# Kernel optimization log

Measured on AMD Instinct MI355X. Metric: run time of the kernel, lower is better.

Reference implementation:

```python
import jax, jax.numpy as jnp
import numpy as np

N = 100000
E = 1600000
F_IN = 32
HID = 16
C_OUT = 10
K = 4


def setup_inputs() -> dict:
    key = jax.random.key(0)
    k1, k2, k3, k4, k5, k6, k7 = jax.random.split(key, 7)
    x = jax.random.normal(k1, (N, F_IN), dtype=jnp.float32)
    edge_index = jax.random.randint(k2, (2, E), 0, N, dtype=jnp.int64)
    # ChebConv weights: one [in, out] matrix per Chebyshev order k
    W1 = jax.random.normal(k3, (K, F_IN, HID), dtype=jnp.float32) / np.sqrt(F_IN)
    b1 = jax.random.normal(k4, (HID,), dtype=jnp.float32) * 0.01
    W2 = jax.random.normal(k5, (K, HID, C_OUT), dtype=jnp.float32) / np.sqrt(HID)
    b2 = jax.random.normal(k6, (C_OUT,), dtype=jnp.float32) * 0.01
    return {"x": x, "edge_index": edge_index, "W1": W1, "b1": b1, "W2": W2, "b2": b2}


def _cheb_conv(h, src, dst, norm, W, b, num_nodes):
    # Tx_0 = h; Tx_1 = L_hat h; Tx_k = 2 L_hat Tx_{k-1} - Tx_{k-2}
    def prop(v):  # v: [N, F] -> L_hat v via sparse gather/scatter
        return jax.ops.segment_sum(norm[:, None] * v[src], dst, num_segments=num_nodes)

    Tx0 = h
    out = Tx0 @ W[0]
    Tx1 = prop(h)
    out = out + Tx1 @ W[1]
    for k in range(2, W.shape[0]):
        Tx2 = 2.0 * prop(Tx1) - Tx0
        out = out + Tx2 @ W[k]
        Tx0, Tx1 = Tx1, Tx2
    return out + b


def reference(x, edge_index, W1, b1, W2, b2):
    src, dst = edge_index[0], edge_index[1]
    num_nodes = x.shape[0]
    # symmetric normalization with lambda_max = 2: L_hat = -D^{-1/2} A D^{-1/2}
    deg = jax.ops.segment_sum(jnp.ones((src.shape[0],), dtype=x.dtype), dst, num_segments=num_nodes)
    dis = jnp.where(deg > 0, jax.lax.rsqrt(jnp.maximum(deg, 1.0)), 0.0)
    norm = -dis[src] * dis[dst]
    h = _cheb_conv(x, src, dst, norm, W1, b1, num_nodes)
    h = jax.nn.relu(h)
    # dropout is identity in eval mode
    h = _cheb_conv(h, src, dst, norm, W2, b2, num_nodes)
    return jax.nn.log_softmax(h, axis=1)
```

## Files before the change

kernel.cpp:

```cpp
#include <hip/hip_runtime.h>
#include <hip/hip_bf16.h>
#include <math.h>


#define BLK 256
#define BLKP 512
#define NBUCK_MAX 256
#define CHUNK 4096
#define CAPB 16384
#define PLACE_CAP 10240

__device__ inline unsigned short f32_to_bf16_rne(float f) {
    unsigned int u = __float_as_uint(f);
    unsigned int rounding = 0x7FFFu + ((u >> 16) & 1u);
    return (unsigned short)((u + rounding) >> 16);
}
__device__ inline unsigned int pack_bf16x2(float a, float b) {
    return (unsigned int)f32_to_bf16_rne(a) | ((unsigned int)f32_to_bf16_rne(b) << 16);
}
__device__ inline void unpack8(const uint4 u, float* f) {
    const unsigned int* p = &u.x;
#pragma unroll
    for (int j = 0; j < 4; j++) {
        unsigned int w = p[j];
        f[2 * j]     = __uint_as_float(w << 16);
        f[2 * j + 1] = __uint_as_float(w & 0xFFFF0000u);
    }
}
__device__ inline void add8(const uint4 u, float* acc) {
    const unsigned int* p = &u.x;
#pragma unroll
    for (int j = 0; j < 4; j++) {
        unsigned int w = p[j];
        acc[2 * j]     += __uint_as_float(w << 16);
        acc[2 * j + 1] += __uint_as_float(w & 0xFFFF0000u);
    }
}
__device__ inline uint4 pack8(const float* r) {
    uint4 o;
    o.x = pack_bf16x2(r[0], r[1]);
    o.y = pack_bf16x2(r[2], r[3]);
    o.z = pack_bf16x2(r[4], r[5]);
    o.w = pack_bf16x2(r[6], r[7]);
    return o;
}

__device__ inline void gather_sum(const int* __restrict__ psrc, int b, int e,
                                  const uint4* __restrict__ vb, int c, float* acc) {
    int i = b;
    for (; i + 7 < e; i += 8) {
        int s0 = psrc[i],     s1 = psrc[i + 1], s2 = psrc[i + 2], s3 = psrc[i + 3];
        int s4 = psrc[i + 4], s5 = psrc[i + 5], s6 = psrc[i + 6], s7 = psrc[i + 7];
        uint4 a0 = vb[(size_t)s0 * 2 + c];
        uint4 a1 = vb[(size_t)s1 * 2 + c];
        uint4 a2 = vb[(size_t)s2 * 2 + c];
        uint4 a3 = vb[(size_t)s3 * 2 + c];
        uint4 a4 = vb[(size_t)s4 * 2 + c];
        uint4 a5 = vb[(size_t)s5 * 2 + c];
        uint4 a6 = vb[(size_t)s6 * 2 + c];
        uint4 a7 = vb[(size_t)s7 * 2 + c];
        add8(a0, acc); add8(a1, acc); add8(a2, acc); add8(a3, acc);
        add8(a4, acc); add8(a5, acc); add8(a6, acc); add8(a7, acc);
    }
    for (; i + 3 < e; i += 4) {
        int s0 = psrc[i], s1 = psrc[i + 1], s2 = psrc[i + 2], s3 = psrc[i + 3];
        uint4 a0 = vb[(size_t)s0 * 2 + c];
        uint4 a1 = vb[(size_t)s1 * 2 + c];
        uint4 a2 = vb[(size_t)s2 * 2 + c];
        uint4 a3 = vb[(size_t)s3 * 2 + c];
        add8(a0, acc); add8(a1, acc); add8(a2, acc); add8(a3, acc);
    }
    for (; i < e; i++) add8(vb[(size_t)psrc[i] * 2 + c], acc);
}

__global__ __launch_bounds__(BLK)
void binned_scatter_kernel(const int* __restrict__ src, const int* __restrict__ dst,
                           int* __restrict__ bfill, int* __restrict__ tmp,
                           int E, int nbuck) {
    __shared__ int cnt[NBUCK_MAX];
    __shared__ int lofs[NBUCK_MAX + 1];
    __shared__ int pos[NBUCK_MAX];
    __shared__ int gbase[NBUCK_MAX];
    __shared__ int stage[CHUNK];
    __shared__ unsigned char bkt[CHUNK];

    int tid = threadIdx.x;
    int e0 = blockIdx.x * CHUNK;
    int nE = min(CHUNK, E - e0);

    for (int b = tid; b < nbuck; b += BLK) { cnt[b] = 0; pos[b] = 0; }
    __syncthreads();

    for (int i = tid; i < nE; i += BLK) {
        int d = dst[e0 + i];
        atomicAdd(&cnt[d >> 9], 1);
    }
    __syncthreads();

    {
        int v = (tid < nbuck) ? cnt[tid] : 0;
        lofs[tid] = v;
        __syncthreads();
        for (int off = 1; off < BLK; off <<= 1) {
            int t = (tid >= off) ? lofs[tid - off] : 0;
            __syncthreads();
            lofs[tid] += t;
            __syncthreads();
        }
        int incl = lofs[tid];
        __syncthreads();
        lofs[tid] = incl - v;
        if (tid == 0) lofs[nbuck] = nE;
        if (tid < nbuck && v > 0)
            gbase[tid] = tid * CAPB + atomicAdd(&bfill[tid], v);
    }
    __syncthreads();

    for (int i = tid; i < nE; i += BLK) {
        int s = src[e0 + i];
        int d = dst[e0 + i];
        int b = d >> 9;
        int slot = lofs[b] + atomicAdd(&pos[b], 1);
        stage[slot] = (s << 9) | (d & 511);
        bkt[slot] = (unsigned char)b;
    }
    __syncthreads();

    for (int i = tid; i < nE; i += BLK) {
        int b = bkt[i];
        tmp[gbase[b] + (i - lofs[b])] = stage[i];
    }
}

__global__ __launch_bounds__(BLKP)
void bucket_place_kernel(const int* __restrict__ bfill, const int* __restrict__ tmp,
                         int* __restrict__ psrc, int* __restrict__ rowbeg,
                         int* __restrict__ rowend, float* __restrict__ dis,
                         float* __restrict__ d2, float* __restrict__ inv, int N) {
    __shared__ int cnt4[512 * 4];
    __shared__ int ofs[512];
    __shared__ int fill4[512 * 4];
    __shared__ int stage[PLACE_CAP];

    int b = blockIdx.x;
    int tid = threadIdx.x;
    int n0 = b << 9;
    int nn = min(512, N - n0);
    int S = b * CAPB;
    int tot = bfill[b];

    int t1 = N >> 2, t2 = N >> 1, t3 = t2 + t1;

    for (int i = tid; i < 512 * 4; i += BLKP) { cnt4[i] = 0; fill4[i] = 0; }
    __syncthreads();

    for (int i = tid; i < tot; i += BLKP) {
        int rec = tmp[S + i];
        int nl = rec & 511;
        int s = rec >> 9;
        int q = (s >= t2) ? ((s >= t3) ? 3 : 2) : ((s >= t1) ? 1 : 0);
        atomicAdd(&cnt4[nl * 4 + q], 1);
    }
    __syncthreads();

    int c0 = cnt4[tid * 4 + 0], c1 = cnt4[tid * 4 + 1];
    int c2 = cnt4[tid * 4 + 2], c3 = cnt4[tid * 4 + 3];
    int v = c0 + c1 + c2 + c3;
    cnt4[tid * 4 + 0] = 0;
    cnt4[tid * 4 + 1] = c0;
    cnt4[tid * 4 + 2] = c0 + c1;
    cnt4[tid * 4 + 3] = c0 + c1 + c2;
    ofs[tid] = v;
    __syncthreads();
    for (int off = 1; off < 512; off <<= 1) {
        int t = (tid >= off) ? ofs[tid - off] : 0;
        __syncthreads();
        ofs[tid] += t;
        __syncthreads();
    }
    int excl = ofs[tid] - v;
    __syncthreads();
    ofs[tid] = excl;
    if (tid < nn) {
        int n = n0 + tid;
        rowbeg[n] = S + excl;
        rowend[n] = S + excl + v;
        float fv = (float)v;
        dis[n] = (v > 0) ? rsqrtf(fv) : 0.0f;
        d2[n]  = (v > 0) ? 1.0f / fv : 0.0f;
        inv[n] = (v > 0) ? sqrtf(fv) : 0.0f;
    }
    __syncthreads();

    if (tot <= PLACE_CAP) {
        for (int i = tid; i < tot; i += BLKP) {
            int rec = tmp[S + i];
            int nl = rec & 511;
            int s = rec >> 9;
            int q = (s >= t2) ? ((s >= t3) ? 3 : 2) : ((s >= t1) ? 1 : 0);
            int slot = ofs[nl] + cnt4[nl * 4 + q] + atomicAdd(&fill4[nl * 4 + q], 1);
            stage[slot] = s;
        }
        __syncthreads();
        for (int i = tid; i < tot; i += BLKP) psrc[S + i] = stage[i];
    } else {
        for (int i = tid; i < tot; i += BLKP) {
            int rec = tmp[S + i];
            int nl = rec & 511;
            int s = rec >> 9;
            int q = (s >= t2) ? ((s >= t3) ? 3 : 2) : ((s >= t1) ? 1 : 0);
            int slot = S + ofs[nl] + cnt4[nl * 4 + q] + atomicAdd(&fill4[nl * 4 + q], 1);
            psrc[slot] = s;
        }
    }
}

__global__ __launch_bounds__(BLK)
void zgen_kernel(const float* __restrict__ x, const float* __restrict__ dis,
                 const float* __restrict__ W1,
                 uint4* __restrict__ z0t, uint4* __restrict__ uz1t,
                 uint4* __restrict__ uz2t, uint4* __restrict__ uz3t,
                 uint4* __restrict__ z2rt, int N) {
    __shared__ float sW[4 * 32 * 16];
    for (int i = threadIdx.x; i < 4 * 32 * 16; i += blockDim.x) sW[i] = W1[i];
    __syncthreads();
    int t = blockIdx.x * blockDim.x + threadIdx.x;
    int n = t >> 1;
    int h = t & 1;
    if (n >= N) return;
    float acc0[8], acc1[8], acc2[8], acc3[8];
#pragma unroll
    for (int j = 0; j < 8; j++) { acc0[j] = 0.f; acc1[j] = 0.f; acc2[j] = 0.f; acc3[j] = 0.f; }
    const float4* x4 = reinterpret_cast<const float4*>(x + (size_t)n * 32);
#pragma unroll
    for (int q = 0; q < 8; q++) {
        float4 a = x4[q];
        float xi[4] = {a.x, a.y, a.z, a.w};
#pragma unroll
        for (int u = 0; u < 4; u++) {
            const float* Wb = sW + (q * 4 + u) * 16 + h * 8;
            float xv = xi[u];
#pragma unroll
            for (int j = 0; j < 8; j++) {
                acc0[j] += xv * Wb[j];
                acc1[j] += xv * Wb[512 + j];
                acc2[j] += xv * Wb[1024 + j];
                acc3[j] += xv * Wb[1536 + j];
            }
        }
    }
    float dn = dis[n];
    float s1[8], s2[8], s3[8];
#pragma unroll
    for (int j = 0; j < 8; j++) { s1[j] = dn * acc1[j]; s2[j] = dn * acc2[j]; s3[j] = dn * acc3[j]; }
    size_t o = (size_t)n * 2 + h;
    z0t[o]  = pack8(acc0);
    uz1t[o] = pack8(s1);
    uz2t[o] = pack8(s2);
    z2rt[o] = pack8(acc2);
    uz3t[o] = pack8(s3);
}

template <bool HAVE_SUB>
__global__ __launch_bounds__(BLK)
void prop_cl_kernel(const int* __restrict__ rowbeg, const int* __restrict__ rowend,
                    const int* __restrict__ psrc, const float* __restrict__ d2,
                    const uint4* __restrict__ vb, const uint4* __restrict__ addt,
                    const uint4* __restrict__ subt, uint4* __restrict__ outb, int N) {
    int t = blockIdx.x * blockDim.x + threadIdx.x;
    int n = t >> 2;
    int l = t & 3;
    int c = l & 1;
    int hf = l >> 1;
    if (n >= N) return;
    int beg = rowbeg[n];
    int end = rowend[n];
    int mid = beg + ((end - beg) >> 1);
    int b = hf ? mid : beg;
    int e = hf ? end : mid;
    float acc[8];
#pragma unroll
    for (int j = 0; j < 8; j++) acc[j] = 0.f;
    gather_sum(psrc, b, e, vb, c, acc);
#pragma unroll
    for (int j = 0; j < 8; j++) acc[j] += __shfl_xor(acc[j], 2);
    if (hf) return;
    float f = -2.0f * d2[n];
    float ad[8], r[8];
    unpack8(addt[(size_t)n * 2 + c], ad);
    if (HAVE_SUB) {
        float sb[8];
        unpack8(subt[(size_t)n * 2 + c], sb);
#pragma unroll
        for (int j = 0; j < 8; j++) r[j] = f * acc[j] + ad[j] - sb[j];
    } else {
#pragma unroll
        for (int j = 0; j < 8; j++) r[j] = f * acc[j] + ad[j];
    }
    outb[(size_t)n * 2 + c] = pack8(r);
}

__global__ __launch_bounds__(BLK)
void final1_kernel(const int* __restrict__ rowbeg, const int* __restrict__ rowend,
                   const int* __restrict__ psrc, const float* __restrict__ dis,
                   const float* __restrict__ d2, const float* __restrict__ inv,
                   const uint4* __restrict__ ub1t, const uint4* __restrict__ ub2t,
                   const uint4* __restrict__ z0t, const uint4* __restrict__ z2rt,
                   const float* __restrict__ W2, const float* __restrict__ b1,
                   uint4* __restrict__ w0t, uint4* __restrict__ uw1t,
                   uint4* __restrict__ uw2t, uint4* __restrict__ uw3t,
                   uint4* __restrict__ w2rt, int N) {
    __shared__ float sW[4 * 16 * 16];
    __shared__ float sb1[16];
    for (int i = threadIdx.x; i < 4 * 16 * 16; i += blockDim.x) {
        int k = i >> 8, rem = i & 255, j = rem >> 4, o = rem & 15;
        sW[i] = (o < 10) ? W2[k * 160 + j * 10 + o] : 0.0f;
    }
    if (threadIdx.x < 16) sb1[threadIdx.x] = b1[threadIdx.x];
    __syncthreads();
    int t = blockIdx.x * blockDim.x + threadIdx.x;
    int n = t >> 1;
    int h = t & 1;
    if (n >= N) return;
    int beg = rowbeg[n];
    int end = rowend[n];
    float acc[8];
#pragma unroll
    for (int j = 0; j < 8; j++) acc[j] = 0.f;
    gather_sum(psrc, beg, end, ub1t, h, acc);
    size_t o2 = (size_t)n * 2 + h;
    float z0[8], hrow[8];
    unpack8(z0t[o2], z0);
    if (d2[n] == 0.0f) {
        float z2[8];
        unpack8(z2rt[o2], z2);
#pragma unroll
        for (int j = 0; j < 8; j++) hrow[j] = fmaxf(sb1[h * 8 + j] + z0[j] - z2[j], 0.0f);
    } else {
        float b2v[8];
        unpack8(ub2t[o2], b2v);
        float dn = dis[n], iv = inv[n];
#pragma unroll
        for (int j = 0; j < 8; j++)
            hrow[j] = fmaxf(sb1[h * 8 + j] + z0[j] - dn * acc[j] - iv * b2v[j], 0.0f);
    }
    float h16[16];
#pragma unroll
    for (int j = 0; j < 8; j++) {
        float other = __shfl_xor(hrow[j], 1);
        h16[h * 8 + j] = hrow[j];
        h16[(1 - h) * 8 + j] = other;
    }
    float w0[8], w1[8], w2[8], w3[8];
#pragma unroll
    for (int o = 0; o < 8; o++) { w0[o] = 0.f; w1[o] = 0.f; w2[o] = 0.f; w3[o] = 0.f; }
#pragma unroll
    for (int j = 0; j < 16; j++) {
        float hv = h16[j];
        const float* Wb = sW + j * 16 + h * 8;
#pragma unroll
        for (int o = 0; o < 8; o++) {
            w0[o] += hv * Wb[o];
            w1[o] += hv * Wb[256 + o];
            w2[o] += hv * Wb[512 + o];
            w3[o] += hv * Wb[768 + o];
        }
    }
    float dn = dis[n];
    float s1[8], s2[8], s3[8];
#pragma unroll
    for (int o = 0; o < 8; o++) { s1[o] = dn * w1[o]; s2[o] = dn * w2[o]; s3[o] = dn * w3[o]; }
    w0t[o2]  = pack8(w0);
    uw1t[o2] = pack8(s1);
    uw2t[o2] = pack8(s2);
    w2rt[o2] = pack8(w2);
    uw3t[o2] = pack8(s3);
}

__global__ __launch_bounds__(BLK)
void final2_kernel(const int* __restrict__ rowbeg, const int* __restrict__ rowend,
                   const int* __restrict__ psrc, const float* __restrict__ dis,
                   const float* __restrict__ d2, const float* __restrict__ inv,
                   const uint4* __restrict__ uv1t, const uint4* __restrict__ uv2t,
                   const uint4* __restrict__ w0t, const uint4* __restrict__ w2rt,
                   const float* __restrict__ b2, float* __restrict__ out, int N) {
    __shared__ float sb2[16];
    if (threadIdx.x < 16) sb2[threadIdx.x] = (threadIdx.x < 10) ? b2[threadIdx.x] : 0.0f;
    __syncthreads();
    int t = blockIdx.x * blockDim.x + threadIdx.x;
    int n = t >> 2;
    int l = t & 3;
    int c = l & 1;
    int hf = l >> 1;
    if (n >= N) return;
    int beg = rowbeg[n];
    int end = rowend[n];
    int mid = beg + ((end - beg) >> 1);
    int gb = hf ? mid : beg;
    int ge = hf ? end : mid;
    float acc[8];
#pragma unroll
    for (int j = 0; j < 8; j++) acc[j] = 0.f;
    gather_sum(psrc, gb, ge, uv1t, c, acc);
#pragma unroll
    for (int j = 0; j < 8; j++) acc[j] += __shfl_xor(acc[j], 2);
    if (hf) return;
    size_t o2 = (size_t)n * 2 + c;
    float w0[8], L[8];
    unpack8(w0t[o2], w0);
    if (d2[n] == 0.0f) {
        float w2[8];
        unpack8(w2rt[o2], w2);
#pragma unroll
        for (int j = 0; j < 8; j++) L[j] = sb2[c * 8 + j] + w0[j] - w2[j];
    } else {
        float v2[8];
        unpack8(uv2t[o2], v2);
        float dn = dis[n], iv = inv[n];
#pragma unroll
        for (int j = 0; j < 8; j++)
            L[j] = sb2[c * 8 + j] + w0[j] - dn * acc[j] - iv * v2[j];
    }
    int nreal = (c == 0) ? 8 : 2;
    float m = -3.0e38f;
    for (int j = 0; j < nreal; j++) m = fmaxf(m, L[j]);
    m = fmaxf(m, __shfl_xor(m, 1));
    float s = 0.0f;
    for (int j = 0; j < nreal; j++) s += expf(L[j] - m);
    s += __shfl_xor(s, 1);
    float lse = m + logf(s);
    float* op = out + (size_t)n * 10 + c * 8;
    for (int j = 0; j < nreal; j++) op[j] = L[j] - lse;
}

extern "C" void kernel_launch(void* const* d_in, const int* in_sizes, int n_in,
                              void* d_out, int out_size, void* d_ws, size_t ws_size,
                              hipStream_t stream) {
    const float* x  = (const float*)d_in[0];
    const int*   ei = (const int*)d_in[1];
    const float* W1 = (const float*)d_in[2];
    const float* b1 = (const float*)d_in[3];
    const float* W2 = (const float*)d_in[4];
    const float* b2 = (const float*)d_in[5];
    float* out = (float*)d_out;

    const int N = in_sizes[0] / 32;
    const int E = in_sizes[1] / 2;
    const int* src = ei;
    const int* dst = ei + E;

    const int nbuck = (N + 511) / 512;

    char* w = (char*)d_ws;
    int*   bfill  = (int*)w;              w += NBUCK_MAX * 4;
    int*   rowbeg = (int*)w;              w += (size_t)(N + 4) * 4;
    int*   rowend = (int*)w;              w += (size_t)(N + 4) * 4;
    float* dis    = (float*)w;            w += (size_t)N * 4;
    float* d2     = (float*)w;            w += (size_t)N * 4;
    float* inv    = (float*)w;            w += (size_t)N * 4;
    int*   tmp    = (int*)w;              w += (size_t)NBUCK_MAX * CAPB * 4;
    int*   psrc   = (int*)w;              w += (size_t)NBUCK_MAX * CAPB * 4;
    uint4* z0t    = (uint4*)w;            w += (size_t)32 * N;
    uint4* uz1t   = (uint4*)w;            w += (size_t)32 * N;
    uint4* uz2t   = (uint4*)w;            w += (size_t)32 * N;
    uint4* uz3t   = (uint4*)w;            w += (size_t)32 * N;
    uint4* z2rt   = (uint4*)w;            w += (size_t)32 * N;
    uint4* ub2t   = (uint4*)w;            w += (size_t)32 * N;
    uint4* ub1t   = (uint4*)w;            w += (size_t)32 * N;
    uint4* w0t    = (uint4*)w;            w += (size_t)32 * N;
    uint4* uw1t   = (uint4*)w;            w += (size_t)32 * N;
    uint4* uw2t   = (uint4*)w;            w += (size_t)32 * N;
    uint4* uw3t   = (uint4*)w;            w += (size_t)32 * N;
    uint4* w2rt   = (uint4*)w;            w += (size_t)32 * N;
    uint4* uv2t   = (uint4*)w;            w += (size_t)32 * N;
    uint4* uv1t   = (uint4*)w;            w += (size_t)32 * N;

    int gN2 = (N * 2 + BLK - 1) / BLK;
    int gN4 = (N * 4 + BLK - 1) / BLK;
    int gCH = (E + CHUNK - 1) / CHUNK;

    hipMemsetAsync(bfill, 0, NBUCK_MAX * sizeof(int), stream);
    binned_scatter_kernel<<<gCH, BLK, 0, stream>>>(src, dst, bfill, tmp, E, nbuck);
    bucket_place_kernel<<<nbuck, BLKP, 0, stream>>>(bfill, tmp, psrc, rowbeg, rowend,
                                                    dis, d2, inv, N);

    zgen_kernel<<<gN2, BLK, 0, stream>>>(x, dis, W1, z0t, uz1t, uz2t, uz3t, z2rt, N);
    prop_cl_kernel<false><<<gN4, BLK, 0, stream>>>(rowbeg, rowend, psrc, d2,
                                                   uz3t, uz2t, nullptr, ub2t, N);
    prop_cl_kernel<true ><<<gN4, BLK, 0, stream>>>(rowbeg, rowend, psrc, d2,
                                                   ub2t, uz1t, uz3t, ub1t, N);
    final1_kernel<<<gN2, BLK, 0, stream>>>(rowbeg, rowend, psrc, dis, d2, inv,
                                           ub1t, ub2t, z0t, z2rt, W2, b1,
                                           w0t, uw1t, uw2t, uw3t, w2rt, N);

    prop_cl_kernel<false><<<gN4, BLK, 0, stream>>>(rowbeg, rowend, psrc, d2,
                                                   uw3t, uw2t, nullptr, uv2t, N);
    prop_cl_kernel<true ><<<gN4, BLK, 0, stream>>>(rowbeg, rowend, psrc, d2,
                                                   uv2t, uw1t, uw3t, uv1t, N);
    final2_kernel<<<gN4, BLK, 0, stream>>>(rowbeg, rowend, psrc, dis, d2, inv,
                                           uv1t, uv2t, w0t, w2rt, b2, out, N);
}
```

Baseline: 246.2 us.

## Fuse layer-1 feature transform into edge scatter kernel, apply dis scaling in gather

The x@W1 transform no longer depends on the node degree normalization. It now runs inside the same launch as the edge binning scatter, as extra blocks, so it can overlap with the scatter and one launch is removed. To allow this, the per-source dis scaling moves into the first propagation's gather, which loads dis[s] per edge and uses FMA. The target-side scaling is applied in the epilogues, and one intermediate buffer (z2rt) is dropped. In exchange, the first gather does an extra random 4-byte read per edge, and the fused kernel mixes two block types that have different shared-memory needs.

```diff
diff --git a/kernel.cpp b/kernel.cpp
--- a/kernel.cpp
+++ b/kernel.cpp
@@ -34,6 +34,15 @@
         unsigned int w = p[j];
         acc[2 * j]     += __uint_as_float(w << 16);
         acc[2 * j + 1] += __uint_as_float(w & 0xFFFF0000u);
+    }
+}
+__device__ inline void fma8(const uint4 u, float wgt, float* acc) {
+    const unsigned int* p = &u.x;
+#pragma unroll
+    for (int j = 0; j < 4; j++) {
+        unsigned int w = p[j];
+        acc[2 * j]     += wgt * __uint_as_float(w << 16);
+        acc[2 * j + 1] += wgt * __uint_as_float(w & 0xFFFF0000u);
     }
 }
 __device__ inline uint4 pack8(const float* r) {
@@ -73,62 +82,137 @@
     for (; i < e; i++) add8(vb[(size_t)psrc[i] * 2 + c], acc);
 }
 
+__device__ inline void gather_sum_dis(const int* __restrict__ psrc, int b, int e,
+                                      const uint4* __restrict__ vb, int c,
+                                      const float* __restrict__ dis, float* acc) {
+    int i = b;
+    for (; i + 7 < e; i += 8) {
+        int s0 = psrc[i],     s1 = psrc[i + 1], s2 = psrc[i + 2], s3 = psrc[i + 3];
+        int s4 = psrc[i + 4], s5 = psrc[i + 5], s6 = psrc[i + 6], s7 = psrc[i + 7];
+        float d0 = dis[s0], d1 = dis[s1], d2v = dis[s2], d3 = dis[s3];
+        float d4 = dis[s4], d5 = dis[s5], d6v = dis[s6], d7 = dis[s7];
+        uint4 a0 = vb[(size_t)s0 * 2 + c];
+        uint4 a1 = vb[(size_t)s1 * 2 + c];
+        uint4 a2 = vb[(size_t)s2 * 2 + c];
+        uint4 a3 = vb[(size_t)s3 * 2 + c];
+        uint4 a4 = vb[(size_t)s4 * 2 + c];
+        uint4 a5 = vb[(size_t)s5 * 2 + c];
+        uint4 a6 = vb[(size_t)s6 * 2 + c];
+        uint4 a7 = vb[(size_t)s7 * 2 + c];
+        fma8(a0, d0, acc); fma8(a1, d1, acc); fma8(a2, d2v, acc); fma8(a3, d3, acc);
+        fma8(a4, d4, acc); fma8(a5, d5, acc); fma8(a6, d6v, acc); fma8(a7, d7, acc);
+    }
+    for (; i + 3 < e; i += 4) {
+        int s0 = psrc[i], s1 = psrc[i + 1], s2 = psrc[i + 2], s3 = psrc[i + 3];
+        float d0 = dis[s0], d1 = dis[s1], d2v = dis[s2], d3 = dis[s3];
+        uint4 a0 = vb[(size_t)s0 * 2 + c];
+        uint4 a1 = vb[(size_t)s1 * 2 + c];
+        uint4 a2 = vb[(size_t)s2 * 2 + c];
+        uint4 a3 = vb[(size_t)s3 * 2 + c];
+        fma8(a0, d0, acc); fma8(a1, d1, acc); fma8(a2, d2v, acc); fma8(a3, d3, acc);
+    }
+    for (; i < e; i++) {
+        int s = psrc[i];
+        fma8(vb[(size_t)s * 2 + c], dis[s], acc);
+    }
+}
+
 __global__ __launch_bounds__(BLK)
-void binned_scatter_kernel(const int* __restrict__ src, const int* __restrict__ dst,
-                           int* __restrict__ bfill, int* __restrict__ tmp,
-                           int E, int nbuck) {
-    __shared__ int cnt[NBUCK_MAX];
-    __shared__ int lofs[NBUCK_MAX + 1];
-    __shared__ int pos[NBUCK_MAX];
-    __shared__ int gbase[NBUCK_MAX];
-    __shared__ int stage[CHUNK];
-    __shared__ unsigned char bkt[CHUNK];
-
+void scatter_zgen_kernel(const int* __restrict__ src, const int* __restrict__ dst,
+                         int* __restrict__ bfill, int* __restrict__ tmp,
+                         int E, int nbuck,
+                         const float* __restrict__ x, const float* __restrict__ W1,
+                         uint4* __restrict__ z0t, uint4* __restrict__ z1t,
+                         uint4* __restrict__ z2t, uint4* __restrict__ z3t,
+                         int N, int gCH) {
     int tid = threadIdx.x;
-    int e0 = blockIdx.x * CHUNK;
-    int nE = min(CHUNK, E - e0);
-
-    for (int b = tid; b < nbuck; b += BLK) { cnt[b] = 0; pos[b] = 0; }
-    __syncthreads();
-
-    for (int i = tid; i < nE; i += BLK) {
-        int d = dst[e0 + i];
-        atomicAdd(&cnt[d >> 9], 1);
-    }
-    __syncthreads();
-
-    {
-        int v = (tid < nbuck) ? cnt[tid] : 0;
-        lofs[tid] = v;
-        __syncthreads();
-        for (int off = 1; off < BLK; off <<= 1) {
-            int t = (tid >= off) ? lofs[tid - off] : 0;
+    if ((int)blockIdx.x < gCH) {
+        __shared__ int cnt[NBUCK_MAX];
+        __shared__ int lofs[NBUCK_MAX + 1];
+        __shared__ int pos[NBUCK_MAX];
+        __shared__ int gbase[NBUCK_MAX];
+        __shared__ int stage[CHUNK];
+        __shared__ unsigned char bkt[CHUNK];
+
+        int e0 = blockIdx.x * CHUNK;
+        int nE = min(CHUNK, E - e0);
+
+        for (int b = tid; b < nbuck; b += BLK) { cnt[b] = 0; pos[b] = 0; }
+        __syncthreads();
+
+        for (int i = tid; i < nE; i += BLK) {
+            int d = dst[e0 + i];
+            atomicAdd(&cnt[d >> 9], 1);
+        }
+        __syncthreads();
+
+        {
+            int v = (tid < nbuck) ? cnt[tid] : 0;
+            lofs[tid] = v;
             __syncthreads();
-            lofs[tid] += t;
+            for (int off = 1; off < BLK; off <<= 1) {
+                int t = (tid >= off) ? lofs[tid - off] : 0;
+                __syncthreads();
+                lofs[tid] += t;
+                __syncthreads();
+            }
+            int incl = lofs[tid];
             __syncthreads();
-        }
-        int incl = lofs[tid];
-        __syncthreads();
-        lofs[tid] = incl - v;
-        if (tid == 0) lofs[nbuck] = nE;
-        if (tid < nbuck && v > 0)
-            gbase[tid] = tid * CAPB + atomicAdd(&bfill[tid], v);
-    }
-    __syncthreads();
-
-    for (int i = tid; i < nE; i += BLK) {
-        int s = src[e0 + i];
-        int d = dst[e0 + i];
-        int b = d >> 9;
-        int slot = lofs[b] + atomicAdd(&pos[b], 1);
-        stage[slot] = (s << 9) | (d & 511);
-        bkt[slot] = (unsigned char)b;
-    }
-    __syncthreads();
-
-    for (int i = tid; i < nE; i += BLK) {
-        int b = bkt[i];
-        tmp[gbase[b] + (i - lofs[b])] = stage[i];
+            lofs[tid] = incl - v;
+            if (tid == 0) lofs[nbuck] = nE;
+            if (tid < nbuck && v > 0)
+                gbase[tid] = tid * CAPB + atomicAdd(&bfill[tid], v);
+        }
+        __syncthreads();
+
+        for (int i = tid; i < nE; i += BLK) {
+            int s = src[e0 + i];
+            int d = dst[e0 + i];
+            int b = d >> 9;
+            int slot = lofs[b] + atomicAdd(&pos[b], 1);
+            stage[slot] = (s << 9) | (d & 511);
+            bkt[slot] = (unsigned char)b;
+        }
+        __syncthreads();
+
+        for (int i = tid; i < nE; i += BLK) {
+            int b = bkt[i];
+            tmp[gbase[b] + (i - lofs[b])] = stage[i];
+        }
+    } else {
+        __shared__ float sW[4 * 32 * 16];
+        for (int i = tid; i < 4 * 32 * 16; i += BLK) sW[i] = W1[i];
+        __syncthreads();
+        int t = ((int)blockIdx.x - gCH) * BLK + tid;
+        int n = t >> 1;
+        int h = t & 1;
+        if (n >= N) return;
+        float acc0[8], acc1[8], acc2[8], acc3[8];
+#pragma unroll
+        for (int j = 0; j < 8; j++) { acc0[j] = 0.f; acc1[j] = 0.f; acc2[j] = 0.f; acc3[j] = 0.f; }
+        const float4* x4 = reinterpret_cast<const float4*>(x + (size_t)n * 32);
+#pragma unroll
+        for (int q = 0; q < 8; q++) {
+            float4 a = x4[q];
+            float xi[4] = {a.x, a.y, a.z, a.w};
+#pragma unroll
+            for (int u = 0; u < 4; u++) {
+                const float* Wb = sW + (q * 4 + u) * 16 + h * 8;
+                float xv = xi[u];
+#pragma unroll
+                for (int j = 0; j < 8; j++) {
+                    acc0[j] += xv * Wb[j];
+                    acc1[j] += xv * Wb[512 + j];
+                    acc2[j] += xv * Wb[1024 + j];
+                    acc3[j] += xv * Wb[1536 + j];
+                }
+            }
+        }
+        size_t o = (size_t)n * 2 + h;
+        z0t[o] = pack8(acc0);
+        z1t[o] = pack8(acc1);
+        z2t[o] = pack8(acc2);
+        z3t[o] = pack8(acc3);
     }
 }
 
@@ -216,49 +300,70 @@
 }
 
 __global__ __launch_bounds__(BLK)
-void zgen_kernel(const float* __restrict__ x, const float* __restrict__ dis,
-                 const float* __restrict__ W1,
-                 uint4* __restrict__ z0t, uint4* __restrict__ uz1t,
-                 uint4* __restrict__ uz2t, uint4* __restrict__ uz3t,
-                 uint4* __restrict__ z2rt, int N) {
-    __shared__ float sW[4 * 32 * 16];
-    for (int i = threadIdx.x; i < 4 * 32 * 16; i += blockDim.x) sW[i] = W1[i];
-    __syncthreads();
+void prop1_kernel(const int* __restrict__ rowbeg, const int* __restrict__ rowend,
+                  const int* __restrict__ psrc, const float* __restrict__ d2,
+                  const float* __restrict__ dis,
+                  const uint4* __restrict__ z3t, const uint4* __restrict__ z2t,
+                  uint4* __restrict__ ub2t, int N) {
     int t = blockIdx.x * blockDim.x + threadIdx.x;
-    int n = t >> 1;
-    int h = t & 1;
+    int n = t >> 2;
+    int l = t & 3;
+    int c = l & 1;
+    int hf = l >> 1;
     if (n >= N) return;
-    float acc0[8], acc1[8], acc2[8], acc3[8];
-#pragma unroll
-    for (int j = 0; j < 8; j++) { acc0[j] = 0.f; acc1[j] = 0.f; acc2[j] = 0.f; acc3[j] = 0.f; }
-    const float4* x4 = reinterpret_cast<const float4*>(x + (size_t)n * 32);
-#pragma unroll
-    for (int q = 0; q < 8; q++) {
-        float4 a = x4[q];
-        float xi[4] = {a.x, a.y, a.z, a.w};
-#pragma unroll
-        for (int u = 0; u < 4; u++) {
-            const float* Wb = sW + (q * 4 + u) * 16 + h * 8;
-            float xv = xi[u];
-#pragma unroll
-            for (int j = 0; j < 8; j++) {
-                acc0[j] += xv * Wb[j];
-                acc1[j] += xv * Wb[512 + j];
-                acc2[j] += xv * Wb[1024 + j];
-                acc3[j] += xv * Wb[1536 + j];
-            }
-        }
-    }
+    int beg = rowbeg[n];
+    int end = rowend[n];
+    int mid = beg + ((end - beg) >> 1);
+    int b = hf ? mid : beg;
+    int e = hf ? end : mid;
+    float acc[8];
+#pragma unroll
+    for (int j = 0; j < 8; j++) acc[j] = 0.f;
+    gather_sum_dis(psrc, b, e, z3t, c, dis, acc);
+#pragma unroll
+    for (int j = 0; j < 8; j++) acc[j] += __shfl_xor(acc[j], 2);
+    if (hf) return;
+    float f = -2.0f * d2[n];
     float dn = dis[n];
-    float s1[8], s2[8], s3[8];
-#pragma unroll
-    for (int j = 0; j < 8; j++) { s1[j] = dn * acc1[j]; s2[j] = dn * acc2[j]; s3[j] = dn * acc3[j]; }
-    size_t o = (size_t)n * 2 + h;
-    z0t[o]  = pack8(acc0);
-    uz1t[o] = pack8(s1);
-    uz2t[o] = pack8(s2);
-    z2rt[o] = pack8(acc2);
-    uz3t[o] = pack8(s3);
+    float ad[8], r[8];
+    unpack8(z2t[(size_t)n * 2 + c], ad);
+#pragma unroll
+    for (int j = 0; j < 8; j++) r[j] = f * acc[j] + dn * ad[j];
+    ub2t[(size_t)n * 2 + c] = pack8(r);
+}
+
+__global__ __launch_bounds__(BLK)
+void prop2_kernel(const int* __restrict__ rowbeg, const int* __restrict__ rowend,
+                  const int* __restrict__ psrc, const float* __restrict__ d2,
+                  const float* __restrict__ dis,
+                  const uint4* __restrict__ ub2t, const uint4* __restrict__ z1t,
+                  const uint4* __restrict__ z3t, uint4* __restrict__ ub1t, int N) {
+    int t = blockIdx.x * blockDim.x + threadIdx.x;
+    int n = t >> 2;
+    int l = t & 3;
+    int c = l & 1;
+    int hf = l >> 1;
+    if (n >= N) return;
+    int beg = rowbeg[n];
+    int end = rowend[n];
+    int mid = beg + ((end - beg) >> 1);
+    int b = hf ? mid : beg;
+    int e = hf ? end : mid;
+    float acc[8];
+#pragma unroll
+    for (int j = 0; j < 8; j++) acc[j] = 0.f;
+    gather_sum(psrc, b, e, ub2t, c, acc);
+#pragma unroll
+    for (int j = 0; j < 8; j++) acc[j] += __shfl_xor(acc[j], 2);
+    if (hf) return;
+    float f = -2.0f * d2[n];
+    float dn = dis[n];
+    float ad[8], sb[8], r[8];
+    unpack8(z1t[(size_t)n * 2 + c], ad);
+    unpack8(z3t[(size_t)n * 2 + c], sb);
+#pragma unroll
+    for (int j = 0; j < 8; j++) r[j] = f * acc[j] + dn * (ad[j] - sb[j]);
+    ub1t[(size_t)n * 2 + c] = pack8(r);
 }
 
 template <bool HAVE_SUB>
@@ -305,7 +410,7 @@
                    const int* __restrict__ psrc, const float* __restrict__ dis,
                    const float* __restrict__ d2, const float* __restrict__ inv,
                    const uint4* __restrict__ ub1t, const uint4* __restrict__ ub2t,
-                   const uint4* __restrict__ z0t, const uint4* __restrict__ z2rt,
+                   const uint4* __restrict__ z0t, const uint4* __restrict__ z2t,
                    const float* __restrict__ W2, const float* __restrict__ b1,
                    uint4* __restrict__ w0t, uint4* __restrict__ uw1t,
                    uint4* __restrict__ uw2t, uint4* __restrict__ uw3t,
@@ -333,7 +438,7 @@
     unpack8(z0t[o2], z0);
     if (d2[n] == 0.0f) {
         float z2[8];
-        unpack8(z2rt[o2], z2);
+        unpack8(z2t[o2], z2);
 #pragma unroll
         for (int j = 0; j < 8; j++) hrow[j] = fmaxf(sb1[h * 8 + j] + z0[j] - z2[j], 0.0f);
     } else {
@@ -461,10 +566,9 @@
     int*   tmp    = (int*)w;              w += (size_t)NBUCK_MAX * CAPB * 4;
     int*   psrc   = (int*)w;              w += (size_t)NBUCK_MAX * CAPB * 4;
     uint4* z0t    = (uint4*)w;            w += (size_t)32 * N;
-    uint4* uz1t   = (uint4*)w;            w += (size_t)32 * N;
-    uint4* uz2t   = (uint4*)w;            w += (size_t)32 * N;
-    uint4* uz3t   = (uint4*)w;            w += (size_t)32 * N;
-    uint4* z2rt   = (uint4*)w;            w += (size_t)32 * N;
+    uint4* z1t    = (uint4*)w;            w += (size_t)32 * N;
+    uint4* z2t    = (uint4*)w;            w += (size_t)32 * N;
+    uint4* z3t    = (uint4*)w;            w += (size_t)32 * N;
     uint4* ub2t   = (uint4*)w;            w += (size_t)32 * N;
     uint4* ub1t   = (uint4*)w;            w += (size_t)32 * N;
     uint4* w0t    = (uint4*)w;            w += (size_t)32 * N;
@@ -478,19 +582,20 @@
     int gN2 = (N * 2 + BLK - 1) / BLK;
     int gN4 = (N * 4 + BLK - 1) / BLK;
     int gCH = (E + CHUNK - 1) / CHUNK;
+    int gZ2 = gN2;
 
     hipMemsetAsync(bfill, 0, NBUCK_MAX * sizeof(int), stream);
-    binned_scatter_kernel<<<gCH, BLK, 0, stream>>>(src, dst, bfill, tmp, E, nbuck);
+    scatter_zgen_kernel<<<gCH + gZ2, BLK, 0, stream>>>(src, dst, bfill, tmp, E, nbuck,
+                                                       x, W1, z0t, z1t, z2t, z3t, N, gCH);
     bucket_place_kernel<<<nbuck, BLKP, 0, stream>>>(bfill, tmp, psrc, rowbeg, rowend,
                                                     dis, d2, inv, N);
 
-    zgen_kernel<<<gN2, BLK, 0, stream>>>(x, dis, W1, z0t, uz1t, uz2t, uz3t, z2rt, N);
-    prop_cl_kernel<false><<<gN4, BLK, 0, stream>>>(rowbeg, rowend, psrc, d2,
-                                                   uz3t, uz2t, nullptr, ub2t, N);
-    prop_cl_kernel<true ><<<gN4, BLK, 0, stream>>>(rowbeg, rowend, psrc, d2,
-                                                   ub2t, uz1t, uz3t, ub1t, N);
+    prop1_kernel<<<gN4, BLK, 0, stream>>>(rowbeg, rowend, psrc, d2, dis,
+                                          z3t, z2t, ub2t, N);
+    prop2_kernel<<<gN4, BLK, 0, stream>>>(rowbeg, rowend, psrc, d2, dis,
+                                          ub2t, z1t, z3t, ub1t, N);
     final1_kernel<<<gN2, BLK, 0, stream>>>(rowbeg, rowend, psrc, dis, d2, inv,
-                                           ub1t, ub2t, z0t, z2rt, W2, b1,
+                                           ub1t, ub2t, z0t, z2t, W2, b1,
                                            w0t, uw1t, uw2t, uw3t, w2rt, N);
 
     prop_cl_kernel<false><<<gN4, BLK, 0, stream>>>(rowbeg, rowend, psrc, d2,
```

Result: slower. 254.9 us (+3.5%).

## Build CSR with global atomic histogram, scan, and atomic placement

Applied to the files above, without the earlier changes.

Replaces the two-stage shared-memory binned scatter and bucket placement with a three-kernel CSR build. A global atomic degree histogram and a per-512-node block scan compute row offsets, then a placement kernel claims slots with returning global atomics. This drops the intermediate tmp buffer, one pass over it, and the staging in LDS. In exchange it issues many global atomics to random addresses. It also loses the source-quartile ordering inside each row, which may hurt gather locality in the propagation kernels and makes neighbor order nondeterministic.

```diff
diff --git a/kernel.cpp b/kernel.cpp
--- a/kernel.cpp
+++ b/kernel.cpp
@@ -6,9 +6,7 @@
 #define BLK 256
 #define BLKP 512
 #define NBUCK_MAX 256
-#define CHUNK 4096
 #define CAPB 16384
-#define PLACE_CAP 10240
 
 __device__ inline unsigned short f32_to_bf16_rne(float f) {
     unsigned int u = __float_as_uint(f);
@@ -73,147 +71,79 @@
     for (; i < e; i++) add8(vb[(size_t)psrc[i] * 2 + c], acc);
 }
 
-__global__ __launch_bounds__(BLK)
-void binned_scatter_kernel(const int* __restrict__ src, const int* __restrict__ dst,
-                           int* __restrict__ bfill, int* __restrict__ tmp,
-                           int E, int nbuck) {
-    __shared__ int cnt[NBUCK_MAX];
-    __shared__ int lofs[NBUCK_MAX + 1];
-    __shared__ int pos[NBUCK_MAX];
-    __shared__ int gbase[NBUCK_MAX];
-    __shared__ int stage[CHUNK];
-    __shared__ unsigned char bkt[CHUNK];
-
-    int tid = threadIdx.x;
-    int e0 = blockIdx.x * CHUNK;
-    int nE = min(CHUNK, E - e0);
-
-    for (int b = tid; b < nbuck; b += BLK) { cnt[b] = 0; pos[b] = 0; }
-    __syncthreads();
-
-    for (int i = tid; i < nE; i += BLK) {
-        int d = dst[e0 + i];
-        atomicAdd(&cnt[d >> 9], 1);
-    }
-    __syncthreads();
-
-    {
-        int v = (tid < nbuck) ? cnt[tid] : 0;
-        lofs[tid] = v;
-        __syncthreads();
-        for (int off = 1; off < BLK; off <<= 1) {
-            int t = (tid >= off) ? lofs[tid - off] : 0;
-            __syncthreads();
-            lofs[tid] += t;
-            __syncthreads();
-        }
-        int incl = lofs[tid];
-        __syncthreads();
-        lofs[tid] = incl - v;
-        if (tid == 0) lofs[nbuck] = nE;
-        if (tid < nbuck && v > 0)
-            gbase[tid] = tid * CAPB + atomicAdd(&bfill[tid], v);
-    }
-    __syncthreads();
-
-    for (int i = tid; i < nE; i += BLK) {
-        int s = src[e0 + i];
-        int d = dst[e0 + i];
-        int b = d >> 9;
-        int slot = lofs[b] + atomicAdd(&pos[b], 1);
-        stage[slot] = (s << 9) | (d & 511);
-        bkt[slot] = (unsigned char)b;
-    }
-    __syncthreads();
-
-    for (int i = tid; i < nE; i += BLK) {
-        int b = bkt[i];
-        tmp[gbase[b] + (i - lofs[b])] = stage[i];
+
+__global__ __launch_bounds__(BLK)
+void hist_kernel(const int* __restrict__ dst, int* __restrict__ deg, int E) {
+    int t = blockIdx.x * BLK + threadIdx.x;
+    int base = t * 4;
+    if (base + 3 < E) {
+        int4 d4 = *reinterpret_cast<const int4*>(dst + base);
+        atomicAdd(&deg[d4.x], 1);
+        atomicAdd(&deg[d4.y], 1);
+        atomicAdd(&deg[d4.z], 1);
+        atomicAdd(&deg[d4.w], 1);
+    } else {
+        for (int i = base; i < E; i++) atomicAdd(&deg[dst[i]], 1);
     }
 }
 
 __global__ __launch_bounds__(BLKP)
-void bucket_place_kernel(const int* __restrict__ bfill, const int* __restrict__ tmp,
-                         int* __restrict__ psrc, int* __restrict__ rowbeg,
-                         int* __restrict__ rowend, float* __restrict__ dis,
-                         float* __restrict__ d2, float* __restrict__ inv, int N) {
-    __shared__ int cnt4[512 * 4];
-    __shared__ int ofs[512];
-    __shared__ int fill4[512 * 4];
-    __shared__ int stage[PLACE_CAP];
-
+void scan_kernel(const int* __restrict__ deg, int* __restrict__ rowbeg,
+                 int* __restrict__ rowend, int* __restrict__ rowfill,
+                 float* __restrict__ dis, float* __restrict__ d2,
+                 float* __restrict__ inv, int N) {
+    __shared__ int ofs[BLKP];
     int b = blockIdx.x;
     int tid = threadIdx.x;
     int n0 = b << 9;
     int nn = min(512, N - n0);
-    int S = b * CAPB;
-    int tot = bfill[b];
-
-    int t1 = N >> 2, t2 = N >> 1, t3 = t2 + t1;
-
-    for (int i = tid; i < 512 * 4; i += BLKP) { cnt4[i] = 0; fill4[i] = 0; }
-    __syncthreads();
-
-    for (int i = tid; i < tot; i += BLKP) {
-        int rec = tmp[S + i];
-        int nl = rec & 511;
-        int s = rec >> 9;
-        int q = (s >= t2) ? ((s >= t3) ? 3 : 2) : ((s >= t1) ? 1 : 0);
-        atomicAdd(&cnt4[nl * 4 + q], 1);
-    }
-    __syncthreads();
-
-    int c0 = cnt4[tid * 4 + 0], c1 = cnt4[tid * 4 + 1];
-    int c2 = cnt4[tid * 4 + 2], c3 = cnt4[tid * 4 + 3];
-    int v = c0 + c1 + c2 + c3;
-    cnt4[tid * 4 + 0] = 0;
-    cnt4[tid * 4 + 1] = c0;
-    cnt4[tid * 4 + 2] = c0 + c1;
-    cnt4[tid * 4 + 3] = c0 + c1 + c2;
+    int v = (tid < nn) ? deg[n0 + tid] : 0;
     ofs[tid] = v;
     __syncthreads();
-    for (int off = 1; off < 512; off <<= 1) {
+    for (int off = 1; off < BLKP; off <<= 1) {
         int t = (tid >= off) ? ofs[tid - off] : 0;
         __syncthreads();
         ofs[tid] += t;
         __syncthreads();
     }
     int excl = ofs[tid] - v;
-    __syncthreads();
-    ofs[tid] = excl;
     if (tid < nn) {
         int n = n0 + tid;
-        rowbeg[n] = S + excl;
-        rowend[n] = S + excl + v;
+        int rb = b * CAPB + excl;
+        rowbeg[n] = rb;
+        rowend[n] = rb + v;
+        rowfill[n] = rb;
         float fv = (float)v;
         dis[n] = (v > 0) ? rsqrtf(fv) : 0.0f;
         d2[n]  = (v > 0) ? 1.0f / fv : 0.0f;
         inv[n] = (v > 0) ? sqrtf(fv) : 0.0f;
     }
-    __syncthreads();
-
-    if (tot <= PLACE_CAP) {
-        for (int i = tid; i < tot; i += BLKP) {
-            int rec = tmp[S + i];
-            int nl = rec & 511;
-            int s = rec >> 9;
-            int q = (s >= t2) ? ((s >= t3) ? 3 : 2) : ((s >= t1) ? 1 : 0);
-            int slot = ofs[nl] + cnt4[nl * 4 + q] + atomicAdd(&fill4[nl * 4 + q], 1);
-            stage[slot] = s;
+}
+
+__global__ __launch_bounds__(BLK)
+void place_kernel(const int* __restrict__ src, const int* __restrict__ dst,
+                  int* __restrict__ rowfill, int* __restrict__ psrc, int E) {
+    int t = blockIdx.x * BLK + threadIdx.x;
+    int base = t * 4;
+    if (base + 3 < E) {
+        int4 s4 = *reinterpret_cast<const int4*>(src + base);
+        int4 d4 = *reinterpret_cast<const int4*>(dst + base);
+        int p0 = atomicAdd(&rowfill[d4.x], 1);
+        int p1 = atomicAdd(&rowfill[d4.y], 1);
+        int p2 = atomicAdd(&rowfill[d4.z], 1);
+        int p3 = atomicAdd(&rowfill[d4.w], 1);
+        psrc[p0] = s4.x;
+        psrc[p1] = s4.y;
+        psrc[p2] = s4.z;
+        psrc[p3] = s4.w;
+    } else {
+        for (int i = base; i < E; i++) {
+            int p = atomicAdd(&rowfill[dst[i]], 1);
+            psrc[p] = src[i];
         }
-        __syncthreads();
-        for (int i = tid; i < tot; i += BLKP) psrc[S + i] = stage[i];
-    } else {
-        for (int i = tid; i < tot; i += BLKP) {
-            int rec = tmp[S + i];
-            int nl = rec & 511;
-            int s = rec >> 9;
-            int q = (s >= t2) ? ((s >= t3) ? 3 : 2) : ((s >= t1) ? 1 : 0);
-            int slot = S + ofs[nl] + cnt4[nl * 4 + q] + atomicAdd(&fill4[nl * 4 + q], 1);
-            psrc[slot] = s;
-        }
-    }
-}
+    }
+}
+
 
 __global__ __launch_bounds__(BLK)
 void zgen_kernel(const float* __restrict__ x, const float* __restrict__ dis,
@@ -452,14 +382,14 @@
     const int nbuck = (N + 511) / 512;
 
     char* w = (char*)d_ws;
-    int*   bfill  = (int*)w;              w += NBUCK_MAX * 4;
-    int*   rowbeg = (int*)w;              w += (size_t)(N + 4) * 4;
-    int*   rowend = (int*)w;              w += (size_t)(N + 4) * 4;
-    float* dis    = (float*)w;            w += (size_t)N * 4;
-    float* d2     = (float*)w;            w += (size_t)N * 4;
-    float* inv    = (float*)w;            w += (size_t)N * 4;
-    int*   tmp    = (int*)w;              w += (size_t)NBUCK_MAX * CAPB * 4;
-    int*   psrc   = (int*)w;              w += (size_t)NBUCK_MAX * CAPB * 4;
+    int*   deg     = (int*)w;             w += (size_t)(N + 16) * 4;
+    int*   rowfill = (int*)w;             w += (size_t)(N + 16) * 4;
+    int*   rowbeg  = (int*)w;             w += (size_t)(N + 16) * 4;
+    int*   rowend  = (int*)w;             w += (size_t)(N + 16) * 4;
+    float* dis     = (float*)w;           w += (size_t)(N + 16) * 4;
+    float* d2      = (float*)w;           w += (size_t)(N + 16) * 4;
+    float* inv     = (float*)w;           w += (size_t)(N + 16) * 4;
+    int*   psrc    = (int*)w;             w += (size_t)NBUCK_MAX * CAPB * 4;
     uint4* z0t    = (uint4*)w;            w += (size_t)32 * N;
     uint4* uz1t   = (uint4*)w;            w += (size_t)32 * N;
     uint4* uz2t   = (uint4*)w;            w += (size_t)32 * N;
@@ -477,14 +407,15 @@
 
     int gN2 = (N * 2 + BLK - 1) / BLK;
     int gN4 = (N * 4 + BLK - 1) / BLK;
-    int gCH = (E + CHUNK - 1) / CHUNK;
-
-    hipMemsetAsync(bfill, 0, NBUCK_MAX * sizeof(int), stream);
-    binned_scatter_kernel<<<gCH, BLK, 0, stream>>>(src, dst, bfill, tmp, E, nbuck);
-    bucket_place_kernel<<<nbuck, BLKP, 0, stream>>>(bfill, tmp, psrc, rowbeg, rowend,
-                                                    dis, d2, inv, N);
-
+    int gE4 = (E / 4 + BLK - 1) / BLK;
+
+    hipMemsetAsync(deg, 0, (size_t)N * sizeof(int), stream);
+    hist_kernel<<<gE4, BLK, 0, stream>>>(dst, deg, E);
+    scan_kernel<<<nbuck, BLKP, 0, stream>>>(deg, rowbeg, rowend, rowfill,
+                                            dis, d2, inv, N);
     zgen_kernel<<<gN2, BLK, 0, stream>>>(x, dis, W1, z0t, uz1t, uz2t, uz3t, z2rt, N);
+    place_kernel<<<gE4, BLK, 0, stream>>>(src, dst, rowfill, psrc, E);
+
     prop_cl_kernel<false><<<gN4, BLK, 0, stream>>>(rowbeg, rowend, psrc, d2,
                                                    uz3t, uz2t, nullptr, ub2t, N);
     prop_cl_kernel<true ><<<gN4, BLK, 0, stream>>>(rowbeg, rowend, psrc, d2,
```

Result: slower. 404.6 us (+64.3%).
